# Performance work log

Measured on AMD Instinct MI355X. Metric: run time of the kernel, lower is better.

## Reference

```python
import jax, jax.numpy as jnp
import numpy as np

N = 100000
IN_C = 128
HID = 128
LAT = 64
E = 800000


def gcn_conv(x, src, dst, norm, W, b, num_nodes):
    # x: [N, Cin]; src/dst: [E+N] (self-loops appended); norm: [E+N]
    xw = x @ W                                   # [N, Cout]
    msg = xw[src] * norm[:, None]                # gather + scale, [E+N, Cout]
    out = jax.ops.segment_sum(msg, dst, num_segments=num_nodes)
    return out + b


def setup_inputs() -> dict:
    key = jax.random.key(0)
    ks = jax.random.split(key, 8)
    x = jax.random.normal(ks[0], (N, IN_C), dtype=jnp.float32)
    edge_index = jax.random.randint(ks[1], (2, E), 0, N, dtype=jnp.int64)
    batch = jnp.zeros((N,), dtype=jnp.int64)
    # GCNConv params (Glorot-ish scale)
    W1 = jax.random.normal(ks[2], (IN_C, HID), dtype=jnp.float32) / np.sqrt(IN_C)
    b1 = jnp.zeros((HID,), dtype=jnp.float32)
    Wmu = jax.random.normal(ks[3], (HID, LAT), dtype=jnp.float32) / np.sqrt(HID)
    bmu = jnp.zeros((LAT,), dtype=jnp.float32)
    Wlv = jax.random.normal(ks[4], (HID, LAT), dtype=jnp.float32) / np.sqrt(HID)
    blv = jnp.zeros((LAT,), dtype=jnp.float32)
    return {"x": x, "edge_index": edge_index, "batch": batch,
            "W1": W1, "b1": b1, "Wmu": Wmu, "bmu": bmu, "Wlv": Wlv, "blv": blv}


def reference(x, edge_index, batch, W1, b1, Wmu, bmu, Wlv, blv):
    num_nodes = x.shape[0]
    loop = jnp.arange(num_nodes, dtype=edge_index.dtype)
    src = jnp.concatenate([edge_index[0], loop])   # source nodes (+self loops)
    dst = jnp.concatenate([edge_index[1], loop])   # target nodes (+self loops)
    # symmetric GCN normalization: deg over targets, norm = d[src]^-1/2 * d[dst]^-1/2
    deg = jax.ops.segment_sum(jnp.ones_like(dst, dtype=x.dtype), dst,
                              num_segments=num_nodes)
    dis = jnp.where(deg > 0, jax.lax.rsqrt(deg), 0.0)
    norm = dis[src] * dis[dst]                      # [E+N]

    h = jax.nn.relu(gcn_conv(x, src, dst, norm, W1, b1, num_nodes))
    mu = gcn_conv(h, src, dst, norm, Wmu, bmu, num_nodes)
    logvar = gcn_conv(h, src, dst, norm, Wlv, blv, num_nodes)
    return (mu, logvar)
```

## Files before the change

kernel.cpp:

```cpp
#include <hip/hip_runtime.h>

typedef short bf16x8 __attribute__((ext_vector_type(8)));
typedef float f32x4 __attribute__((ext_vector_type(4)));

#define ELLK 32
#define OCAP 4096
#define CSTRIDE 16

static __device__ __forceinline__ float4 f4zero() { return make_float4(0.f, 0.f, 0.f, 0.f); }

static __device__ __forceinline__ unsigned short f2bf(float f) {
  unsigned u = __float_as_uint(f);
  u += 0x7FFFu + ((u >> 16) & 1u);
  return (unsigned short)(u >> 16);
}
static __device__ __forceinline__ float2 bf2x2(unsigned u) {
  float2 r;
  r.x = __uint_as_float(u << 16);
  r.y = __uint_as_float(u & 0xFFFF0000u);
  return r;
}

__global__ void k_setup(const float* __restrict__ W1, const float* __restrict__ Wmu,
                        const float* __restrict__ Wlv, unsigned short* __restrict__ Wt1,
                        unsigned short* __restrict__ Wt2, uint4* __restrict__ cntz,
                        int* __restrict__ ocount, unsigned* __restrict__ A,
                        unsigned* __restrict__ H, int nz4, int nbz, int n) {
  int b = blockIdx.x;
  if (b < nbz) {
    int i = b * 256 + threadIdx.x;
    if (i < nz4) cntz[i] = make_uint4(0u, 0u, 0u, 0u);
    if (b == 0) {
      int t = threadIdx.x;
      if (t == 0) *ocount = 0;
      if (t < 64) A[(size_t)n * 64 + t] = 0u;
      else if (t < 128) H[(size_t)n * 64 + (t - 64)] = 0u;
    }
  } else {
    int id = (b - nbz) * 256 + threadIdx.x;
    if (id < 16384) {
      int j = id & 7, lane = (id >> 3) & 63, g = id >> 9;
      int kk = g >> 3, nt = g & 7, li = lane & 15, quad = lane >> 4;
      int nn = nt * 16 + li, k = kk * 32 + quad * 8 + j;
      Wt1[id] = f2bf(W1[k * 128 + nn]);
    } else {
      int id2 = id - 16384;
      int j = id2 & 7, lane = (id2 >> 3) & 63, g = id2 >> 9;
      int kk = g >> 3, nt = g & 7, li = lane & 15, quad = lane >> 4;
      int nn = nt * 16 + li, k = kk * 32 + quad * 8 + j;
      float v = (nn < 64) ? Wmu[k * 64 + nn] : Wlv[k * 64 + (nn - 64)];
      Wt2[id2] = f2bf(v);
    }
  }
}

__global__ void k_fill(const int* __restrict__ ei, int* __restrict__ cnt,
                       int* __restrict__ ell, int2* __restrict__ ovf,
                       int* __restrict__ ocount, int E, int n) {
  int e0 = blockIdx.x * 1024 + threadIdx.x;
  int ss[4], dd[4], pos[4];
  bool ok[4];
#pragma unroll
  for (int k = 0; k < 4; ++k) {
    int e = e0 + k * 256;
    ok[k] = (e < E);
    ss[k] = ok[k] ? ei[e] : 0;
    dd[k] = ok[k] ? ei[E + e] : 0;
  }
#pragma unroll
  for (int k = 0; k < 4; ++k)
    pos[k] = ok[k] ? atomicAdd(&cnt[(size_t)dd[k] * CSTRIDE], 1) : ELLK;
#pragma unroll
  for (int k = 0; k < 4; ++k) {
    if (!ok[k]) continue;
    if (pos[k] < ELLK) {
      __builtin_nontemporal_store(ss[k], &ell[(size_t)pos[k] * n + dd[k]]);
    } else {
      int o = atomicAdd(ocount, 1);
      if (o < OCAP) ovf[o] = make_int2(dd[k], ss[k]);
    }
  }
}

__global__ __launch_bounds__(256, 4) void k_gemm1(
    const float* __restrict__ x, const unsigned short* __restrict__ Wt,
    const int* __restrict__ cnt, unsigned short* __restrict__ A,
    float* __restrict__ dnorm, unsigned* __restrict__ mflag, int n) {
  __shared__ unsigned short Xl[64 * 136];
  __shared__ float dnl[64];
  const int tid = threadIdx.x;
  const int row0 = blockIdx.x * 64;
  {
#pragma unroll
    for (int i = 0; i < 8; ++i) {
      int idx = tid + i * 256;
      int r = idx >> 5, c = idx & 31;
      int gi = row0 + r;
      float4 v = (gi < n) ? ((const float4*)x)[(size_t)gi * 32 + c] : f4zero();
      ushort4 p;
      p.x = f2bf(v.x); p.y = f2bf(v.y); p.z = f2bf(v.z); p.w = f2bf(v.w);
      *(ushort4*)&Xl[r * 136 + c * 4] = p;
    }
  }
  if (tid < 64) {
    int gi = row0 + tid;
    float dn = 0.f;
    if (gi < n) {
      int c = cnt[(size_t)gi * CSTRIDE];
      dn = rsqrtf((float)(c + 1));
      dnorm[gi] = dn;
      int mm = (c < ELLK) ? c : ELLK;
      mflag[gi] = (unsigned)mm | ((c > ELLK) ? 0x80000000u : 0u);
    }
    dnl[tid] = dn;
  }
  __syncthreads();

  const int wave = tid >> 6, lane = tid & 63;
  const int li = lane & 15, quad = lane >> 4;
  const int m0 = wave * 16;
  const bf16x8* Wf = (const bf16x8*)Wt;
  f32x4 acc[8];
#pragma unroll
  for (int t = 0; t < 8; ++t) acc[t] = (f32x4){0.f, 0.f, 0.f, 0.f};

#pragma unroll
  for (int kk = 0; kk < 4; ++kk) {
    int ko = kk * 32 + quad * 8;
    bf16x8 a = *(const bf16x8*)&Xl[(m0 + li) * 136 + ko];
    bf16x8 bf[8];
#pragma unroll
    for (int nt = 0; nt < 8; ++nt) bf[nt] = Wf[(kk * 8 + nt) * 64 + lane];
#pragma unroll
    for (int nt = 0; nt < 8; ++nt)
      acc[nt] = __builtin_amdgcn_mfma_f32_16x16x32_bf16(a, bf[nt], acc[nt], 0, 0, 0);
  }
  __syncthreads();
  float dn[4];
#pragma unroll
  for (int r = 0; r < 4; ++r) dn[r] = dnl[m0 + quad * 4 + r];
#pragma unroll
  for (int nt = 0; nt < 8; ++nt)
#pragma unroll
    for (int r = 0; r < 4; ++r)
      Xl[(m0 + quad * 4 + r) * 136 + nt * 16 + li] = f2bf(acc[nt][r] * dn[r]);
  __syncthreads();
  {
    uint4* A4 = (uint4*)A;
#pragma unroll
    for (int i = 0; i < 4; ++i) {
      int idx = tid + i * 256;
      int r = idx >> 4, c = idx & 15;
      int gi = row0 + r;
      if (gi < n) A4[(size_t)gi * 16 + c] = *(uint4*)&Xl[r * 136 + c * 8];
    }
  }
}

__global__ __launch_bounds__(256) void k_spmm1(
    const unsigned* __restrict__ mflag, const float* __restrict__ dnorm,
    const int* __restrict__ ell, const int2* __restrict__ ovf,
    const int* __restrict__ ocount, const unsigned* __restrict__ S,
    unsigned* __restrict__ D, const float2* __restrict__ bias, int n) {
  int wid = (blockIdx.x * blockDim.x + threadIdx.x) >> 6;
  if (wid >= n) return;
  int lane = threadIdx.x & 63;

  unsigned mf = mflag[wid];
  int m = (int)(mf & 0xFFFFu);
  float dsd = dnorm[wid];
  float2 acc = bf2x2(S[(size_t)wid * 64 + lane]);

  const int* ep = ell + wid;
  int nbt = (m + 7) >> 3;
  for (int b = 0; b < nbt; ++b) {
    int j0 = b * 8;
    int idx[8];
#pragma unroll
    for (int k = 0; k < 8; ++k) idx[k] = ep[(size_t)(j0 + k) * n];
#pragma unroll
    for (int k = 0; k < 8; ++k) idx[k] = (j0 + k < m) ? idx[k] : n;
    unsigned u[8];
#pragma unroll
    for (int k = 0; k < 8; ++k) u[k] = S[(size_t)idx[k] * 64 + lane];
#pragma unroll
    for (int k = 0; k < 8; ++k) {
      float2 f = bf2x2(u[k]);
      acc.x += f.x;
      acc.y += f.y;
    }
  }
  if (mf & 0x80000000u) {
    int oc = *ocount;
    if (oc > OCAP) oc = OCAP;
    for (int k = 0; k < oc; ++k) {
      int2 e = ovf[k];
      if (e.x == wid) {
        float2 u0 = bf2x2(S[(size_t)e.y * 64 + lane]);
        acc.x += u0.x;
        acc.y += u0.y;
      }
    }
  }
  float2 b = bias[lane];
  float2 o;
  o.x = dsd * fmaxf(fmaf(dsd, acc.x, b.x), 0.f);
  o.y = dsd * fmaxf(fmaf(dsd, acc.y, b.y), 0.f);
  unsigned pk = (unsigned)f2bf(o.x) | ((unsigned)f2bf(o.y) << 16);
  D[(size_t)wid * 64 + lane] = pk;
}

__global__ __launch_bounds__(256, 4) void k_spmm2_gemm2(
    const unsigned* __restrict__ mflag, const float* __restrict__ dnorm,
    const int* __restrict__ ell, const int2* __restrict__ ovf,
    const int* __restrict__ ocount, const unsigned* __restrict__ H,
    const unsigned short* __restrict__ Wt, const float* __restrict__ bmu,
    const float* __restrict__ blv, float* __restrict__ out, int n) {
  __shared__ unsigned short Xl[64 * 136];
  const int tid = threadIdx.x;
  const int wave = tid >> 6, lane = tid & 63;
  const int row0 = blockIdx.x * 64;

#pragma unroll 1
  for (int i = 0; i < 16; ++i) {
    int nd = row0 + wave * 16 + i;
    unsigned pk = 0u;
    if (nd < n) {
      unsigned mf = mflag[nd];
      int m = (int)(mf & 0xFFFFu);
      float dsd = dnorm[nd];
      float2 acc = bf2x2(H[(size_t)nd * 64 + lane]);
      const int* ep = ell + nd;
      int nbt = (m + 7) >> 3;
      for (int b = 0; b < nbt; ++b) {
        int j0 = b * 8;
        int idx[8];
#pragma unroll
        for (int k = 0; k < 8; ++k) idx[k] = ep[(size_t)(j0 + k) * n];
#pragma unroll
        for (int k = 0; k < 8; ++k) idx[k] = (j0 + k < m) ? idx[k] : n;
        unsigned u[8];
#pragma unroll
        for (int k = 0; k < 8; ++k) u[k] = H[(size_t)idx[k] * 64 + lane];
#pragma unroll
        for (int k = 0; k < 8; ++k) {
          float2 f = bf2x2(u[k]);
          acc.x += f.x;
          acc.y += f.y;
        }
      }
      if (mf & 0x80000000u) {
        int oc = *ocount;
        if (oc > OCAP) oc = OCAP;
        for (int k = 0; k < oc; ++k) {
          int2 e = ovf[k];
          if (e.x == nd) {
            float2 u0 = bf2x2(H[(size_t)e.y * 64 + lane]);
            acc.x += u0.x;
            acc.y += u0.y;
          }
        }
      }
      float2 o;
      o.x = dsd * acc.x;
      o.y = dsd * acc.y;
      pk = (unsigned)f2bf(o.x) | ((unsigned)f2bf(o.y) << 16);
    }
    *(unsigned*)&Xl[(wave * 16 + i) * 136 + 2 * lane] = pk;
  }
  __syncthreads();

  const int li = lane & 15, quad = lane >> 4;
  const int m0 = wave * 16;
  const bf16x8* Wf = (const bf16x8*)Wt;

  float bias[8];
#pragma unroll
  for (int nt = 0; nt < 8; ++nt) {
    int c = nt * 16 + li;
    bias[nt] = (c < 64) ? bmu[c] : blv[c - 64];
  }

  f32x4 acc[8];
#pragma unroll
  for (int t = 0; t < 8; ++t) acc[t] = (f32x4){0.f, 0.f, 0.f, 0.f};

#pragma unroll
  for (int kk = 0; kk < 4; ++kk) {
    int ko = kk * 32 + quad * 8;
    bf16x8 a = *(const bf16x8*)&Xl[(m0 + li) * 136 + ko];
    bf16x8 bf[8];
#pragma unroll
    for (int nt = 0; nt < 8; ++nt) bf[nt] = Wf[(kk * 8 + nt) * 64 + lane];
#pragma unroll
    for (int nt = 0; nt < 8; ++nt)
      acc[nt] = __builtin_amdgcn_mfma_f32_16x16x32_bf16(a, bf[nt], acc[nt], 0, 0, 0);
  }
#pragma unroll
  for (int nt = 0; nt < 8; ++nt) {
    int col = nt * 16 + li;
#pragma unroll
    for (int r = 0; r < 4; ++r) {
      int gi = row0 + m0 + quad * 4 + r;
      if (gi < n) {
        float v = acc[nt][r] + bias[nt];
        if (col < 64) out[(size_t)gi * 64 + col] = v;
        else          out[(size_t)(n + gi) * 64 + (col - 64)] = v;
      }
    }
  }
}

extern "C" void kernel_launch(void* const* d_in, const int* in_sizes, int n_in,
                              void* d_out, int out_size, void* d_ws, size_t ws_size,
                              hipStream_t stream) {
  const float* x   = (const float*)d_in[0];
  const int*   ei  = (const int*)d_in[1];
  const float* W1  = (const float*)d_in[3];
  const float* b1  = (const float*)d_in[4];
  const float* Wmu = (const float*)d_in[5];
  const float* bmu = (const float*)d_in[6];
  const float* Wlv = (const float*)d_in[7];
  const float* blv = (const float*)d_in[8];
  float* out = (float*)d_out;

  const int n = in_sizes[0] / 128;
  const int E = in_sizes[1] / 2;

  float* ws = (float*)d_ws;
  size_t p = 0;
  int* cnt    = (int*)(ws + p); p += (size_t)n * CSTRIDE;
  int* ocount = (int*)(ws + p); p += 1;
  p = (p + 3) & ~(size_t)3;
  int* ell    = (int*)(ws + p); p += (size_t)n * ELLK;
  int2* ovf   = (int2*)(ws + p); p += (size_t)OCAP * 2;
  unsigned* A = (unsigned*)(ws + p); p += (size_t)(n + 1) * 64;
  unsigned* H = (unsigned*)(ws + p); p += (size_t)(n + 1) * 64;
  unsigned short* Wt1 = (unsigned short*)(ws + p); p += 8192;
  unsigned short* Wt2 = (unsigned short*)(ws + p); p += 8192;
  float* dnorm    = (float*)(ws + p); p += n;
  unsigned* mflag = (unsigned*)(ws + p); p += n;

  int nz4  = (n * CSTRIDE) / 4;
  int nbz  = (nz4 + 255) / 256;
  int eb   = (E + 1023) / 1024;
  int gblk = (n + 63) / 64;
  int sblk = (n + 3) / 4;

  k_setup<<<nbz + 128, 256, 0, stream>>>(W1, Wmu, Wlv, Wt1, Wt2, (uint4*)cnt, ocount,
                                         A, H, nz4, nbz, n);
  k_fill<<<eb, 256, 0, stream>>>(ei, cnt, ell, ovf, ocount, E, n);
  k_gemm1<<<gblk, 256, 0, stream>>>(x, Wt1, cnt, (unsigned short*)A, dnorm, mflag, n);
  k_spmm1<<<sblk, 256, 0, stream>>>(mflag, dnorm, ell, ovf, ocount, A, H,
                                    (const float2*)b1, n);
  k_spmm2_gemm2<<<gblk, 256, 0, stream>>>(mflag, dnorm, ell, ovf, ocount, H, Wt2,
                                          bmu, blv, out, n);
}
```

Before: 282.6 us.

## Fuse all five GCN stages into one cooperative persistent kernel with grid syncs

Adds a persistent cooperative kernel that runs setup, edge fill, GEMM1, SpMM1 and the fused SpMM2+GEMM2 in a fixed 1024-block grid, with grid-wide syncs between stages and grid-stride loops over work. It removes the separate kernel launches and their inter-kernel gaps. The trade-offs are a fixed grid size that may not match per-stage parallelism, grid.sync overhead, and register and shared-memory pressure from one large kernel, which can lower occupancy. If the cooperative launch fails, the code falls back to the original multi-kernel path.

```diff
diff --git a/kernel.cpp b/kernel.cpp
--- a/kernel.cpp
+++ b/kernel.cpp
@@ -1,4 +1,7 @@
 #include <hip/hip_runtime.h>
+#include <hip/hip_cooperative_groups.h>
+
+namespace cg = cooperative_groups;
 
 typedef short bf16x8 __attribute__((ext_vector_type(8)));
 typedef float f32x4 __attribute__((ext_vector_type(4)));
@@ -6,6 +9,7 @@
 #define ELLK 32
 #define OCAP 4096
 #define CSTRIDE 16
+#define MGRID 1024
 
 static __device__ __forceinline__ float4 f4zero() { return make_float4(0.f, 0.f, 0.f, 0.f); }
 
@@ -19,6 +23,262 @@
   r.x = __uint_as_float(u << 16);
   r.y = __uint_as_float(u & 0xFFFF0000u);
   return r;
+}
+
+__global__ __launch_bounds__(256, 4) void k_mega(
+    const float* __restrict__ x, const int* __restrict__ ei,
+    const float* __restrict__ W1, const float* __restrict__ Wmu,
+    const float* __restrict__ Wlv, const float2* __restrict__ b1,
+    const float* __restrict__ bmu, const float* __restrict__ blv,
+    float* __restrict__ out, int* __restrict__ cnt, int* __restrict__ ocount,
+    int* __restrict__ ell, int2* __restrict__ ovf, unsigned* __restrict__ A,
+    unsigned* __restrict__ H, unsigned short* __restrict__ Wt1,
+    unsigned short* __restrict__ Wt2, float* __restrict__ dnorm,
+    unsigned* __restrict__ mflag, int n, int E, int nz4, int gblk) {
+  cg::grid_group grid = cg::this_grid();
+  __shared__ unsigned short Xl[64 * 136];
+  __shared__ float dnl[64];
+  const int tid = threadIdx.x;
+  const int gtid = blockIdx.x * 256 + tid;
+  const int gth = gridDim.x * 256;
+  const int wave = tid >> 6, lane = tid & 63;
+  const int li = lane & 15, quad = lane >> 4;
+  const int m0 = wave * 16;
+
+  {
+    uint4* cntz = (uint4*)cnt;
+    for (int i = gtid; i < nz4; i += gth) cntz[i] = make_uint4(0u, 0u, 0u, 0u);
+    if (gtid == 0) *ocount = 0;
+    if (gtid < 64) A[(size_t)n * 64 + gtid] = 0u;
+    else if (gtid < 128) H[(size_t)n * 64 + (gtid - 64)] = 0u;
+    for (int id = gtid; id < 32768; id += gth) {
+      if (id < 16384) {
+        int j = id & 7, ln = (id >> 3) & 63, g = id >> 9;
+        int kk = g >> 3, nt = g & 7, lli = ln & 15, qq = ln >> 4;
+        int nn = nt * 16 + lli, k = kk * 32 + qq * 8 + j;
+        Wt1[id] = f2bf(W1[k * 128 + nn]);
+      } else {
+        int id2 = id - 16384;
+        int j = id2 & 7, ln = (id2 >> 3) & 63, g = id2 >> 9;
+        int kk = g >> 3, nt = g & 7, lli = ln & 15, qq = ln >> 4;
+        int nn = nt * 16 + lli, k = kk * 32 + qq * 8 + j;
+        float v = (nn < 64) ? Wmu[k * 64 + nn] : Wlv[k * 64 + (nn - 64)];
+        Wt2[id2] = f2bf(v);
+      }
+    }
+  }
+  grid.sync();
+
+  for (int e = gtid; e < E; e += gth) {
+    int s = ei[e];
+    int d = ei[E + e];
+    int pos = atomicAdd(&cnt[(size_t)d * CSTRIDE], 1);
+    if (pos < ELLK) {
+      __builtin_nontemporal_store(s, &ell[(size_t)pos * n + d]);
+    } else {
+      int o = atomicAdd(ocount, 1);
+      if (o < OCAP) ovf[o] = make_int2(d, s);
+    }
+  }
+  grid.sync();
+
+  for (int t = blockIdx.x; t < gblk; t += gridDim.x) {
+    const int row0 = t * 64;
+#pragma unroll
+    for (int i = 0; i < 8; ++i) {
+      int idx = tid + i * 256;
+      int r = idx >> 5, c = idx & 31;
+      int gi = row0 + r;
+      float4 v = (gi < n) ? ((const float4*)x)[(size_t)gi * 32 + c] : f4zero();
+      ushort4 p;
+      p.x = f2bf(v.x); p.y = f2bf(v.y); p.z = f2bf(v.z); p.w = f2bf(v.w);
+      *(ushort4*)&Xl[r * 136 + c * 4] = p;
+    }
+    if (tid < 64) {
+      int gi = row0 + tid;
+      float dn = 0.f;
+      if (gi < n) {
+        int c = cnt[(size_t)gi * CSTRIDE];
+        dn = rsqrtf((float)(c + 1));
+        dnorm[gi] = dn;
+        int mm = (c < ELLK) ? c : ELLK;
+        mflag[gi] = (unsigned)mm | ((c > ELLK) ? 0x80000000u : 0u);
+      }
+      dnl[tid] = dn;
+    }
+    __syncthreads();
+
+    const bf16x8* Wf = (const bf16x8*)Wt1;
+    f32x4 acc[8];
+#pragma unroll
+    for (int q = 0; q < 8; ++q) acc[q] = (f32x4){0.f, 0.f, 0.f, 0.f};
+#pragma unroll
+    for (int kk = 0; kk < 4; ++kk) {
+      int ko = kk * 32 + quad * 8;
+      bf16x8 a = *(const bf16x8*)&Xl[(m0 + li) * 136 + ko];
+      bf16x8 bf[8];
+#pragma unroll
+      for (int nt = 0; nt < 8; ++nt) bf[nt] = Wf[(kk * 8 + nt) * 64 + lane];
+#pragma unroll
+      for (int nt = 0; nt < 8; ++nt)
+        acc[nt] = __builtin_amdgcn_mfma_f32_16x16x32_bf16(a, bf[nt], acc[nt], 0, 0, 0);
+    }
+    __syncthreads();
+    float dn[4];
+#pragma unroll
+    for (int r = 0; r < 4; ++r) dn[r] = dnl[m0 + quad * 4 + r];
+#pragma unroll
+    for (int nt = 0; nt < 8; ++nt)
+#pragma unroll
+      for (int r = 0; r < 4; ++r)
+        Xl[(m0 + quad * 4 + r) * 136 + nt * 16 + li] = f2bf(acc[nt][r] * dn[r]);
+    __syncthreads();
+    {
+      uint4* A4 = (uint4*)A;
+#pragma unroll
+      for (int i = 0; i < 4; ++i) {
+        int idx = tid + i * 256;
+        int r = idx >> 4, c = idx & 15;
+        int gi = row0 + r;
+        if (gi < n) A4[(size_t)gi * 16 + c] = *(uint4*)&Xl[r * 136 + c * 8];
+      }
+    }
+    __syncthreads();
+  }
+  grid.sync();
+
+  for (int wid = blockIdx.x * 4 + wave; wid < n; wid += gridDim.x * 4) {
+    unsigned mf = mflag[wid];
+    int m = (int)(mf & 0xFFFFu);
+    float dsd = dnorm[wid];
+    float2 acc = bf2x2(A[(size_t)wid * 64 + lane]);
+    const int* ep = ell + wid;
+    int nbt = (m + 7) >> 3;
+    for (int b = 0; b < nbt; ++b) {
+      int j0 = b * 8;
+      int idx[8];
+#pragma unroll
+      for (int k = 0; k < 8; ++k) idx[k] = ep[(size_t)(j0 + k) * n];
+#pragma unroll
+      for (int k = 0; k < 8; ++k) idx[k] = (j0 + k < m) ? idx[k] : n;
+      unsigned u[8];
+#pragma unroll
+      for (int k = 0; k < 8; ++k) u[k] = A[(size_t)idx[k] * 64 + lane];
+#pragma unroll
+      for (int k = 0; k < 8; ++k) {
+        float2 f = bf2x2(u[k]);
+        acc.x += f.x;
+        acc.y += f.y;
+      }
+    }
+    if (mf & 0x80000000u) {
+      int oc = *ocount;
+      if (oc > OCAP) oc = OCAP;
+      for (int k = 0; k < oc; ++k) {
+        int2 e = ovf[k];
+        if (e.x == wid) {
+          float2 u0 = bf2x2(A[(size_t)e.y * 64 + lane]);
+          acc.x += u0.x;
+          acc.y += u0.y;
+        }
+      }
+    }
+    float2 b = b1[lane];
+    float2 o;
+    o.x = dsd * fmaxf(fmaf(dsd, acc.x, b.x), 0.f);
+    o.y = dsd * fmaxf(fmaf(dsd, acc.y, b.y), 0.f);
+    unsigned pk = (unsigned)f2bf(o.x) | ((unsigned)f2bf(o.y) << 16);
+    H[(size_t)wid * 64 + lane] = pk;
+  }
+  grid.sync();
+
+  for (int t = blockIdx.x; t < gblk; t += gridDim.x) {
+    const int row0 = t * 64;
+#pragma unroll 1
+    for (int i = 0; i < 16; ++i) {
+      int nd = row0 + wave * 16 + i;
+      unsigned pk = 0u;
+      if (nd < n) {
+        unsigned mf = mflag[nd];
+        int m = (int)(mf & 0xFFFFu);
+        float dsd = dnorm[nd];
+        float2 acc = bf2x2(H[(size_t)nd * 64 + lane]);
+        const int* ep = ell + nd;
+        int nbt = (m + 7) >> 3;
+        for (int b = 0; b < nbt; ++b) {
+          int j0 = b * 8;
+          int idx[8];
+#pragma unroll
+          for (int k = 0; k < 8; ++k) idx[k] = ep[(size_t)(j0 + k) * n];
+#pragma unroll
+          for (int k = 0; k < 8; ++k) idx[k] = (j0 + k < m) ? idx[k] : n;
+          unsigned u[8];
+#pragma unroll
+          for (int k = 0; k < 8; ++k) u[k] = H[(size_t)idx[k] * 64 + lane];
+#pragma unroll
+          for (int k = 0; k < 8; ++k) {
+            float2 f = bf2x2(u[k]);
+            acc.x += f.x;
+            acc.y += f.y;
+          }
+        }
+        if (mf & 0x80000000u) {
+          int oc = *ocount;
+          if (oc > OCAP) oc = OCAP;
+          for (int k = 0; k < oc; ++k) {
+            int2 e = ovf[k];
+            if (e.x == nd) {
+              float2 u0 = bf2x2(H[(size_t)e.y * 64 + lane]);
+              acc.x += u0.x;
+              acc.y += u0.y;
+            }
+          }
+        }
+        float2 o;
+        o.x = dsd * acc.x;
+        o.y = dsd * acc.y;
+        pk = (unsigned)f2bf(o.x) | ((unsigned)f2bf(o.y) << 16);
+      }
+      *(unsigned*)&Xl[(wave * 16 + i) * 136 + 2 * lane] = pk;
+    }
+    __syncthreads();
+
+    const bf16x8* Wf = (const bf16x8*)Wt2;
+    float bias[8];
+#pragma unroll
+    for (int nt = 0; nt < 8; ++nt) {
+      int c = nt * 16 + li;
+      bias[nt] = (c < 64) ? bmu[c] : blv[c - 64];
+    }
+    f32x4 acc[8];
+#pragma unroll
+    for (int q = 0; q < 8; ++q) acc[q] = (f32x4){0.f, 0.f, 0.f, 0.f};
+#pragma unroll
+    for (int kk = 0; kk < 4; ++kk) {
+      int ko = kk * 32 + quad * 8;
+      bf16x8 a = *(const bf16x8*)&Xl[(m0 + li) * 136 + ko];
+      bf16x8 bf[8];
+#pragma unroll
+      for (int nt = 0; nt < 8; ++nt) bf[nt] = Wf[(kk * 8 + nt) * 64 + lane];
+#pragma unroll
+      for (int nt = 0; nt < 8; ++nt)
+        acc[nt] = __builtin_amdgcn_mfma_f32_16x16x32_bf16(a, bf[nt], acc[nt], 0, 0, 0);
+    }
+#pragma unroll
+    for (int nt = 0; nt < 8; ++nt) {
+      int col = nt * 16 + li;
+#pragma unroll
+      for (int r = 0; r < 4; ++r) {
+        int gi = row0 + m0 + quad * 4 + r;
+        if (gi < n) {
+          float v = acc[nt][r] + bias[nt];
+          if (col < 64) out[(size_t)gi * 64 + col] = v;
+          else          out[(size_t)(n + gi) * 64 + (col - 64)] = v;
+        }
+      }
+    }
+    __syncthreads();
+  }
 }
 
 __global__ void k_setup(const float* __restrict__ W1, const float* __restrict__ Wmu,
@@ -123,7 +383,6 @@
   f32x4 acc[8];
 #pragma unroll
   for (int t = 0; t < 8; ++t) acc[t] = (f32x4){0.f, 0.f, 0.f, 0.f};
-
 #pragma unroll
   for (int kk = 0; kk < 4; ++kk) {
     int ko = kk * 32 + quad * 8;
@@ -165,12 +424,10 @@
   int wid = (blockIdx.x * blockDim.x + threadIdx.x) >> 6;
   if (wid >= n) return;
   int lane = threadIdx.x & 63;
-
   unsigned mf = mflag[wid];
   int m = (int)(mf & 0xFFFFu);
   float dsd = dnorm[wid];
   float2 acc = bf2x2(S[(size_t)wid * 64 + lane]);
-
   const int* ep = ell + wid;
   int nbt = (m + 7) >> 3;
   for (int b = 0; b < nbt; ++b) {
@@ -220,7 +477,6 @@
   const int tid = threadIdx.x;
   const int wave = tid >> 6, lane = tid & 63;
   const int row0 = blockIdx.x * 64;
-
 #pragma unroll 1
   for (int i = 0; i < 16; ++i) {
     int nd = row0 + wave * 16 + i;
@@ -273,18 +529,15 @@
   const int li = lane & 15, quad = lane >> 4;
   const int m0 = wave * 16;
   const bf16x8* Wf = (const bf16x8*)Wt;
-
   float bias[8];
 #pragma unroll
   for (int nt = 0; nt < 8; ++nt) {
     int c = nt * 16 + li;
     bias[nt] = (c < 64) ? bmu[c] : blv[c - 64];
   }
-
   f32x4 acc[8];
 #pragma unroll
   for (int t = 0; t < 8; ++t) acc[t] = (f32x4){0.f, 0.f, 0.f, 0.f};
-
 #pragma unroll
   for (int kk = 0; kk < 4; ++kk) {
     int ko = kk * 32 + quad * 8;
@@ -347,6 +600,28 @@
   int gblk = (n + 63) / 64;
   int sblk = (n + 3) / 4;
 
+  static int coop = -1;
+  if (coop < 0) {
+    int dev = 0, v = 0;
+    (void)hipGetDevice(&dev);
+    if (hipDeviceGetAttribute(&v, hipDeviceAttributeCooperativeLaunch, dev) != hipSuccess) v = 0;
+    coop = v;
+  }
+
+  if (coop) {
+    const float2* b1f2 = (const float2*)b1;
+    void* args[] = {(void*)&x,   (void*)&ei,   (void*)&W1,  (void*)&Wmu, (void*)&Wlv,
+                    (void*)&b1f2,(void*)&bmu,  (void*)&blv, (void*)&out, (void*)&cnt,
+                    (void*)&ocount, (void*)&ell, (void*)&ovf, (void*)&A, (void*)&H,
+                    (void*)&Wt1, (void*)&Wt2, (void*)&dnorm, (void*)&mflag,
+                    (void*)&n, (void*)&E, (void*)&nz4, (void*)&gblk};
+    hipError_t err = hipLaunchCooperativeKernel((void*)k_mega, dim3(MGRID), dim3(256),
+                                                args, 0, stream);
+    if (err == hipSuccess) return;
+    (void)hipGetLastError();
+    coop = 0;
+  }
+
   k_setup<<<nbz + 128, 256, 0, stream>>>(W1, Wmu, Wlv, Wt1, Wt2, (uint4*)cnt, ocount,
                                          A, H, nz4, nbz, n);
   k_fill<<<eb, 256, 0, stream>>>(ei, cnt, ell, ovf, ocount, E, n);
```

Result: no change. 282.0 us (-0.2%).
